# Performance work log

Measured on AMD Instinct MI355X. Metric: run time of the kernel, lower is better.

The kernel has to match this reference:

```python
import jax, jax.numpy as jnp
import numpy as np

D_MODEL = 1024
NUM_HEADS = 16
HEAD_DIM = D_MODEL // NUM_HEADS

def setup_inputs() -> dict:
    key = jax.random.key(0)
    ks = jax.random.split(key, 9)
    B, L = 2, 2048
    s = 1.0 / np.sqrt(D_MODEL)
    return {
        "x":  jax.random.normal(ks[0], (B, L, D_MODEL), dtype=jnp.float32),
        "Wq": jax.random.uniform(ks[1], (D_MODEL, D_MODEL), jnp.float32, -s, s),
        "bq": jax.random.uniform(ks[2], (D_MODEL,), jnp.float32, -s, s),
        "Wk": jax.random.uniform(ks[3], (D_MODEL, D_MODEL), jnp.float32, -s, s),
        "bk": jax.random.uniform(ks[4], (D_MODEL,), jnp.float32, -s, s),
        "Wv": jax.random.uniform(ks[5], (D_MODEL, D_MODEL), jnp.float32, -s, s),
        "bv": jax.random.uniform(ks[6], (D_MODEL,), jnp.float32, -s, s),
        "Wo": jax.random.uniform(ks[7], (D_MODEL, D_MODEL), jnp.float32, -s, s),
        "bo": jax.random.uniform(ks[8], (D_MODEL,), jnp.float32, -s, s),
    }

def _split_heads(t):
    B, L, _ = t.shape
    return t.reshape(B, L, NUM_HEADS, HEAD_DIM).transpose(0, 2, 1, 3)  # [B,H,L,Dh]

def reference(x, Wq, bq, Wk, bk, Wv, bv, Wo, bo):
    # Linear projections (torch Linear: y = x @ W.T + b)
    Q = _split_heads(x @ Wq.T + bq)
    K = _split_heads(x @ Wk.T + bk)
    V = _split_heads(x @ Wv.T + bv)
    scale = 1.0 / jnp.sqrt(jnp.asarray(HEAD_DIM, dtype=x.dtype))
    scores = jnp.einsum('bhqd,bhkd->bhqk', Q, K) * scale  # [B,H,L,L]
    attn_weights = jax.nn.softmax(scores, axis=-1)
    ctx = jnp.einsum('bhqk,bhkd->bhqd', attn_weights, V)  # [B,H,L,Dh]
    B, H, L, Dh = ctx.shape
    ctx = ctx.transpose(0, 2, 1, 3).reshape(B, L, H * Dh)
    out = ctx @ Wo.T + bo  # dropout p=0.0 -> identity
    return (out, attn_weights)
```

## Files before the change

### kernel.cpp

```cpp
#include <hip/hip_runtime.h>

typedef unsigned short u16;
typedef __bf16 bf16x8 __attribute__((ext_vector_type(8)));
typedef float f32x4 __attribute__((ext_vector_type(4)));

#define LSTR 40
#define WSTR 72

__device__ __forceinline__ u16 f2bf(float f) {
    union { float f; unsigned int u; } v; v.f = f;
    unsigned int u = v.u;
    u += 0x7fffu + ((u >> 16) & 1u);
    return (u16)(u >> 16);
}

__device__ __forceinline__ u16 cvt_bf(float f) {
    __bf16 h = (__bf16)f;
    union { __bf16 h; u16 u; } v; v.h = h; return v.u;
}

__device__ __forceinline__ void stage8_bf(const u16* __restrict__ g, u16* __restrict__ lds) {
    *(uint4*)lds = *(const uint4*)g;
}

__device__ __forceinline__ void gload16(const u16* g, u16* l) {
    __builtin_amdgcn_global_load_lds((const __attribute__((address_space(1))) unsigned int*)(const void*)g,
                                     (__attribute__((address_space(3))) unsigned int*)(void*)l, 16, 0, 0);
}

__device__ __forceinline__ void mfma_tile(const u16* lA, const u16* lB,
                                          int wm, int wn, int quad, int m16,
                                          f32x4 (&acc)[2][2]) {
    bf16x8 a0 = *(const bf16x8*)(lA + (wm + m16) * LSTR + quad * 8);
    bf16x8 a1 = *(const bf16x8*)(lA + (wm + 16 + m16) * LSTR + quad * 8);
    bf16x8 b0 = *(const bf16x8*)(lB + (wn + m16) * LSTR + quad * 8);
    bf16x8 b1 = *(const bf16x8*)(lB + (wn + 16 + m16) * LSTR + quad * 8);
    acc[0][0] = __builtin_amdgcn_mfma_f32_16x16x32_bf16(a0, b0, acc[0][0], 0, 0, 0);
    acc[0][1] = __builtin_amdgcn_mfma_f32_16x16x32_bf16(a0, b1, acc[0][1], 0, 0, 0);
    acc[1][0] = __builtin_amdgcn_mfma_f32_16x16x32_bf16(a1, b0, acc[1][0], 0, 0, 0);
    acc[1][1] = __builtin_amdgcn_mfma_f32_16x16x32_bf16(a1, b1, acc[1][1], 0, 0, 0);
}

__global__ __launch_bounds__(256) void k_cvtX(const float* __restrict__ src, u16* __restrict__ dst) {
    const size_t i = ((size_t)blockIdx.x * 256 + threadIdx.x) * 8;
    float4 v0 = *(const float4*)(src + i);
    float4 v1 = *(const float4*)(src + i + 4);
    u16 o[8];
    o[0] = f2bf(v0.x); o[1] = f2bf(v0.y); o[2] = f2bf(v0.z); o[3] = f2bf(v0.w);
    o[4] = f2bf(v1.x); o[5] = f2bf(v1.y); o[6] = f2bf(v1.z); o[7] = f2bf(v1.w);
    *(uint4*)(dst + i) = *(const uint4*)o;
}

__global__ __launch_bounds__(256) void k_cvtW(const float* __restrict__ w0, const float* __restrict__ w1,
                                              const float* __restrict__ w2, const float* __restrict__ w3,
                                              u16* __restrict__ dst) {
    const int z = blockIdx.z;
    const float* src = z == 0 ? w0 : z == 1 ? w1 : z == 2 ? w2 : w3;
    const size_t i = ((size_t)blockIdx.x * 256 + threadIdx.x) * 8;
    float4 v0 = *(const float4*)(src + i);
    float4 v1 = *(const float4*)(src + i + 4);
    u16 o[8];
    o[0] = f2bf(v0.x); o[1] = f2bf(v0.y); o[2] = f2bf(v0.z); o[3] = f2bf(v0.w);
    o[4] = f2bf(v1.x); o[5] = f2bf(v1.y); o[6] = f2bf(v1.z); o[7] = f2bf(v1.w);
    *(uint4*)(dst + (size_t)z * 1048576 + i) = *(const uint4*)o;
}

__global__ __launch_bounds__(256) void k_qkv(const u16* __restrict__ Xb, const u16* __restrict__ Wb,
                                             const float* __restrict__ bq, const float* __restrict__ bk,
                                             const float* __restrict__ bv,
                                             u16* __restrict__ Q, u16* __restrict__ Kd, u16* __restrict__ Vt) {
    __shared__ __align__(16) u16 lA[128 * 32];
    __shared__ __align__(16) u16 lB[128 * 32];
    const int t = threadIdx.x;
    const int n0 = blockIdx.x * 128;
    const int m0 = blockIdx.y * 128;
    const int lane = t & 63, wave = t >> 6;
    const int wm = (wave >> 1) * 64, wn = (wave & 1) * 64;
    const int quad = lane >> 4, m16 = lane & 15;
    const int r4 = t >> 2, c8 = (t & 3) * 8;
    f32x4 acc[4][4] = {};
    for (int k0 = 0; k0 < 1024; k0 += 32) {
        gload16(Xb + (size_t)(m0 + r4) * 1024 + k0 + c8,       &lA[t * 8]);
        gload16(Xb + (size_t)(m0 + 64 + r4) * 1024 + k0 + c8,  &lA[2048 + t * 8]);
        gload16(Wb + (size_t)(n0 + r4) * 1024 + k0 + c8,       &lB[t * 8]);
        gload16(Wb + (size_t)(n0 + 64 + r4) * 1024 + k0 + c8,  &lB[2048 + t * 8]);
        __syncthreads();
        bf16x8 af[4], bfr[4];
#pragma unroll
        for (int i = 0; i < 4; ++i) {
            af[i]  = *(const bf16x8*)(lA + (wm + i * 16 + m16) * 32 + quad * 8);
            bfr[i] = *(const bf16x8*)(lB + (wn + i * 16 + m16) * 32 + quad * 8);
        }
#pragma unroll
        for (int mi = 0; mi < 4; ++mi)
#pragma unroll
            for (int ni = 0; ni < 4; ++ni)
                acc[mi][ni] = __builtin_amdgcn_mfma_f32_16x16x32_bf16(af[mi], bfr[ni], acc[mi][ni], 0, 0, 0);
        __syncthreads();
    }
#pragma unroll
    for (int ni = 0; ni < 4; ++ni) {
        const int gcol = n0 + wn + ni * 16 + m16;
        const int mat = gcol >> 10;
        const int col = gcol & 1023;
        const int h = col >> 6, d = col & 63;
        const float bias = (mat == 0 ? bq : mat == 1 ? bk : bv)[col];
        u16* dst = mat == 0 ? Q : mat == 1 ? Kd : Vt;
#pragma unroll
        for (int mi = 0; mi < 4; ++mi)
#pragma unroll
            for (int e = 0; e < 4; ++e) {
                const int row = m0 + wm + mi * 16 + quad * 4 + e;
                const int b = row >> 11, l = row & 2047;
                const float v = acc[mi][ni][e] + bias;
                size_t idx;
                if (mat == 2) idx = (((size_t)(b * 16 + h)) * 64 + d) * 2048 + l;
                else          idx = (((size_t)(b * 16 + h)) * 2048 + l) * 64 + d;
                dst[idx] = cvt_bf(v);
            }
    }
}

__global__ __launch_bounds__(256) void k_attn(const u16* __restrict__ Q,
                                              const u16* __restrict__ K,
                                              const u16* __restrict__ Vt,
                                              float* __restrict__ attn,
                                              u16* __restrict__ ctx) {
    __shared__ __align__(16) u16 lK[64 * WSTR];
    __shared__ __align__(16) u16 lV[64 * WSTR];
    __shared__ __align__(16) u16 lW[64 * WSTR];
    __shared__ float sred[2][64];
    const int t = threadIdx.x;
    const int bh = blockIdx.y;
    const int m0 = blockIdx.x * 64;
    const int lane = t & 63, wave = t >> 6;
    const int wm = (wave >> 1) * 32, wn = (wave & 1) * 32;
    const int quad = lane >> 4, m16 = lane & 15;
    const int sr = t >> 3, sc = (t & 7) * 8;
    const u16* Qh = Q + (size_t)bh * 2048 * 64;
    const u16* Kh = K + (size_t)bh * 2048 * 64;
    const u16* Vh = Vt + (size_t)bh * 64 * 2048;
    float* ah = attn + ((size_t)bh << 22) + (size_t)m0 * 2048;

    bf16x8 qf[2][2];
#pragma unroll
    for (int mi = 0; mi < 2; ++mi)
#pragma unroll
        for (int ks = 0; ks < 2; ++ks)
            qf[mi][ks] = *(const bf16x8*)(Qh + (size_t)(m0 + wm + mi * 16 + m16) * 64 + ks * 32 + quad * 8);

    float slane[8] = {};

    for (int kt = 0; kt < 32; ++kt) {
        __syncthreads();
        *(uint4*)&lK[sr * WSTR + sc]        = *(const uint4*)(Kh + (size_t)(kt * 64 + sr) * 64 + sc);
        *(uint4*)&lK[(sr + 32) * WSTR + sc] = *(const uint4*)(Kh + (size_t)(kt * 64 + sr + 32) * 64 + sc);
        __syncthreads();
        f32x4 sacc[2][2] = {};
#pragma unroll
        for (int ks = 0; ks < 2; ++ks) {
            bf16x8 b0 = *(const bf16x8*)(lK + (wn + m16) * WSTR + ks * 32 + quad * 8);
            bf16x8 b1 = *(const bf16x8*)(lK + (wn + 16 + m16) * WSTR + ks * 32 + quad * 8);
            sacc[0][0] = __builtin_amdgcn_mfma_f32_16x16x32_bf16(qf[0][ks], b0, sacc[0][0], 0, 0, 0);
            sacc[0][1] = __builtin_amdgcn_mfma_f32_16x16x32_bf16(qf[0][ks], b1, sacc[0][1], 0, 0, 0);
            sacc[1][0] = __builtin_amdgcn_mfma_f32_16x16x32_bf16(qf[1][ks], b0, sacc[1][0], 0, 0, 0);
            sacc[1][1] = __builtin_amdgcn_mfma_f32_16x16x32_bf16(qf[1][ks], b1, sacc[1][1], 0, 0, 0);
        }
#pragma unroll
        for (int mi = 0; mi < 2; ++mi)
#pragma unroll
            for (int e = 0; e < 4; ++e)
                slane[mi * 4 + e] += __expf(sacc[mi][0][e] * 0.125f) + __expf(sacc[mi][1][e] * 0.125f);
    }

#pragma unroll
    for (int i = 0; i < 8; ++i) {
        float s = slane[i];
        s += __shfl_xor(s, 1); s += __shfl_xor(s, 2); s += __shfl_xor(s, 4); s += __shfl_xor(s, 8);
        slane[i] = s;
    }
    if (m16 == 0) {
#pragma unroll
        for (int mi = 0; mi < 2; ++mi)
#pragma unroll
            for (int e = 0; e < 4; ++e)
                sred[wave & 1][wm + mi * 16 + quad * 4 + e] = slane[mi * 4 + e];
    }
    __syncthreads();
    float inv[8];
#pragma unroll
    for (int mi = 0; mi < 2; ++mi)
#pragma unroll
        for (int e = 0; e < 4; ++e) {
            const int row = wm + mi * 16 + quad * 4 + e;
            inv[mi * 4 + e] = 1.0f / (sred[0][row] + sred[1][row]);
        }

    f32x4 cacc[2][2] = {};
    for (int kt = 0; kt < 32; ++kt) {
        __syncthreads();
        *(uint4*)&lK[sr * WSTR + sc]        = *(const uint4*)(Kh + (size_t)(kt * 64 + sr) * 64 + sc);
        *(uint4*)&lK[(sr + 32) * WSTR + sc] = *(const uint4*)(Kh + (size_t)(kt * 64 + sr + 32) * 64 + sc);
        *(uint4*)&lV[sr * WSTR + sc]        = *(const uint4*)(Vh + (size_t)sr * 2048 + kt * 64 + sc);
        *(uint4*)&lV[(sr + 32) * WSTR + sc] = *(const uint4*)(Vh + (size_t)(sr + 32) * 2048 + kt * 64 + sc);
        __syncthreads();
        f32x4 sacc[2][2] = {};
#pragma unroll
        for (int ks = 0; ks < 2; ++ks) {
            bf16x8 b0 = *(const bf16x8*)(lK + (wn + m16) * WSTR + ks * 32 + quad * 8);
            bf16x8 b1 = *(const bf16x8*)(lK + (wn + 16 + m16) * WSTR + ks * 32 + quad * 8);
            sacc[0][0] = __builtin_amdgcn_mfma_f32_16x16x32_bf16(qf[0][ks], b0, sacc[0][0], 0, 0, 0);
            sacc[0][1] = __builtin_amdgcn_mfma_f32_16x16x32_bf16(qf[0][ks], b1, sacc[0][1], 0, 0, 0);
            sacc[1][0] = __builtin_amdgcn_mfma_f32_16x16x32_bf16(qf[1][ks], b0, sacc[1][0], 0, 0, 0);
            sacc[1][1] = __builtin_amdgcn_mfma_f32_16x16x32_bf16(qf[1][ks], b1, sacc[1][1], 0, 0, 0);
        }
#pragma unroll
        for (int mi = 0; mi < 2; ++mi)
#pragma unroll
            for (int ni = 0; ni < 2; ++ni)
#pragma unroll
                for (int e = 0; e < 4; ++e) {
                    const float w = __expf(sacc[mi][ni][e] * 0.125f) * inv[mi * 4 + e];
                    const int row = wm + mi * 16 + quad * 4 + e;
                    const int col = wn + ni * 16 + m16;
                    ah[(size_t)row * 2048 + kt * 64 + col] = w;
                    lW[row * WSTR + col] = cvt_bf(w);
                }
        __syncthreads();
#pragma unroll
        for (int ks = 0; ks < 2; ++ks) {
            bf16x8 a0 = *(const bf16x8*)(lW + (wm + m16) * WSTR + ks * 32 + quad * 8);
            bf16x8 a1 = *(const bf16x8*)(lW + (wm + 16 + m16) * WSTR + ks * 32 + quad * 8);
            bf16x8 b0 = *(const bf16x8*)(lV + (wn + m16) * WSTR + ks * 32 + quad * 8);
            bf16x8 b1 = *(const bf16x8*)(lV + (wn + 16 + m16) * WSTR + ks * 32 + quad * 8);
            cacc[0][0] = __builtin_amdgcn_mfma_f32_16x16x32_bf16(a0, b0, cacc[0][0], 0, 0, 0);
            cacc[0][1] = __builtin_amdgcn_mfma_f32_16x16x32_bf16(a0, b1, cacc[0][1], 0, 0, 0);
            cacc[1][0] = __builtin_amdgcn_mfma_f32_16x16x32_bf16(a1, b0, cacc[1][0], 0, 0, 0);
            cacc[1][1] = __builtin_amdgcn_mfma_f32_16x16x32_bf16(a1, b1, cacc[1][1], 0, 0, 0);
        }
    }

#pragma unroll
    for (int mi = 0; mi < 2; ++mi)
#pragma unroll
        for (int ni = 0; ni < 2; ++ni)
#pragma unroll
            for (int e = 0; e < 4; ++e) {
                const int row = m0 + wm + mi * 16 + quad * 4 + e;
                const int col = wn + ni * 16 + m16;
                ctx[(size_t)bh * 2048 * 64 + (size_t)row * 64 + col] = cvt_bf(cacc[mi][ni][e]);
            }
}

__global__ __launch_bounds__(256) void k_out(const u16* __restrict__ ctx,
                                             const u16* __restrict__ WoB,
                                             const float* __restrict__ bo,
                                             float* __restrict__ out) {
    __shared__ __align__(16) u16 lA[64 * LSTR];
    __shared__ __align__(16) u16 lB[64 * LSTR];
    const int t = threadIdx.x;
    const int n0 = blockIdx.x * 64, m0 = blockIdx.y * 64;
    const int lane = t & 63, wave = t >> 6;
    const int wm = (wave >> 1) * 32, wn = (wave & 1) * 32;
    const int quad = lane >> 4, m16 = lane & 15;
    const int r = t >> 2, c8 = (t & 3) * 8;
    const int m = m0 + r;
    const int b = m >> 11, l = m & 2047;
    f32x4 acc[2][2] = {};
    for (int k0 = 0; k0 < 1024; k0 += 32) {
        const int kk = k0 + c8;
        const int h = kk >> 6, d = kk & 63;
        stage8_bf(ctx + (((size_t)(b * 16 + h) * 2048 + l) * 64 + d), &lA[r * LSTR + c8]);
        stage8_bf(WoB + (size_t)(n0 + r) * 1024 + k0 + c8, &lB[r * LSTR + c8]);
        __syncthreads();
        mfma_tile(lA, lB, wm, wn, quad, m16, acc);
        __syncthreads();
    }
#pragma unroll
    for (int mi = 0; mi < 2; ++mi)
#pragma unroll
        for (int ni = 0; ni < 2; ++ni) {
            const int col = n0 + wn + ni * 16 + m16;
            const float bv = bo[col];
#pragma unroll
            for (int e = 0; e < 4; ++e) {
                const int row = m0 + wm + mi * 16 + quad * 4 + e;
                out[(size_t)row * 1024 + col] = acc[mi][ni][e] + bv;
            }
        }
}

extern "C" void kernel_launch(void* const* d_in, const int* in_sizes, int n_in,
                              void* d_out, int out_size, void* d_ws, size_t ws_size,
                              hipStream_t stream) {
    const float* x  = (const float*)d_in[0];
    const float* Wq = (const float*)d_in[1];
    const float* bq = (const float*)d_in[2];
    const float* Wk = (const float*)d_in[3];
    const float* bk = (const float*)d_in[4];
    const float* Wv = (const float*)d_in[5];
    const float* bv = (const float*)d_in[6];
    const float* Wo = (const float*)d_in[7];
    const float* bo = (const float*)d_in[8];

    float* out_f = (float*)d_out;
    float* attn  = out_f + (size_t)4096 * 1024;

    u16* Xb = (u16*)d_ws;
    u16* Wb = Xb + (size_t)4194304;
    u16* Qb = Wb + (size_t)4194304;
    u16* Kb = Qb + (size_t)4194304;
    u16* Vt = Kb + (size_t)4194304;

    dim3 blk(256);
    k_cvtX<<<dim3(2048), blk, 0, stream>>>(x, Xb);
    k_cvtW<<<dim3(512, 1, 4), blk, 0, stream>>>(Wq, Wk, Wv, Wo, Wb);
    k_qkv<<<dim3(24, 32), blk, 0, stream>>>(Xb, Wb, bq, bk, bv, Qb, Kb, Vt);
    k_attn<<<dim3(32, 32), blk, 0, stream>>>(Qb, Kb, Vt, attn, Qb);
    k_out<<<dim3(16, 64), blk, 0, stream>>>(Qb, Wb + (size_t)3072 * 1024, bo, out_f);
}
```

Measured before the change: 780.3 us.

## Transpose score MFMA so each lane holds four consecutive keys for vector stores

The score MFMA operands are swapped to compute K·Q^T, so each lane's accumulator holds four consecutive key columns of one query row. This lets the fp32 attention-weight writes become 16-byte vector stores and the bf16 LDS writes become 8-byte stores, replacing scattered scalar stores. It also moves the attention store after the barrier, uses exp2 with a folded log2e scale, and simplifies the row-sum reduction to two cross-quad shuffles. Row ownership per wave changes, which adds some index bookkeeping and fixed offset registers.

```diff
diff --git a/kernel.cpp b/kernel.cpp
--- a/kernel.cpp
+++ b/kernel.cpp
@@ -134,6 +134,8 @@
     const int bh = blockIdx.y;
     const int m0 = blockIdx.x * 64;
     const int lane = t & 63, wave = t >> 6;
+    const int wq = (wave & 1) * 32;
+    const int wk = (wave >> 1) * 32;
     const int wm = (wave >> 1) * 32, wn = (wave & 1) * 32;
     const int quad = lane >> 4, m16 = lane & 15;
     const int sr = t >> 3, sc = (t & 7) * 8;
@@ -142,101 +144,120 @@
     const u16* Vh = Vt + (size_t)bh * 64 * 2048;
     float* ah = attn + ((size_t)bh << 22) + (size_t)m0 * 2048;
 
+    const float SC = 0.18033688011112042f;
+
     bf16x8 qf[2][2];
 #pragma unroll
+    for (int ni = 0; ni < 2; ++ni)
+#pragma unroll
+        for (int ks = 0; ks < 2; ++ks)
+            qf[ni][ks] = *(const bf16x8*)(Qh + (size_t)(m0 + wq + ni * 16 + m16) * 64 + ks * 32 + quad * 8);
+
+    float slane[2] = {0.f, 0.f};
+    {
+        const u16* kp = Kh + (size_t)sr * 64 + sc;
+        for (int kt = 0; kt < 32; ++kt) {
+            __syncthreads();
+            *(uint4*)&lK[sr * WSTR + sc]        = *(const uint4*)kp;
+            *(uint4*)&lK[(sr + 32) * WSTR + sc] = *(const uint4*)(kp + 32 * 64);
+            kp += 64 * 64;
+            __syncthreads();
+            f32x4 sacc[2][2] = {};
+#pragma unroll
+            for (int ks = 0; ks < 2; ++ks) {
+                bf16x8 a0 = *(const bf16x8*)(lK + (wk + m16) * WSTR + ks * 32 + quad * 8);
+                bf16x8 a1 = *(const bf16x8*)(lK + (wk + 16 + m16) * WSTR + ks * 32 + quad * 8);
+                sacc[0][0] = __builtin_amdgcn_mfma_f32_16x16x32_bf16(a0, qf[0][ks], sacc[0][0], 0, 0, 0);
+                sacc[0][1] = __builtin_amdgcn_mfma_f32_16x16x32_bf16(a0, qf[1][ks], sacc[0][1], 0, 0, 0);
+                sacc[1][0] = __builtin_amdgcn_mfma_f32_16x16x32_bf16(a1, qf[0][ks], sacc[1][0], 0, 0, 0);
+                sacc[1][1] = __builtin_amdgcn_mfma_f32_16x16x32_bf16(a1, qf[1][ks], sacc[1][1], 0, 0, 0);
+            }
+#pragma unroll
+            for (int mi = 0; mi < 2; ++mi)
+#pragma unroll
+                for (int e = 0; e < 4; ++e) {
+                    slane[0] += __builtin_amdgcn_exp2f(sacc[mi][0][e] * SC);
+                    slane[1] += __builtin_amdgcn_exp2f(sacc[mi][1][e] * SC);
+                }
+        }
+    }
+#pragma unroll
+    for (int ni = 0; ni < 2; ++ni) {
+        slane[ni] += __shfl_xor(slane[ni], 16);
+        slane[ni] += __shfl_xor(slane[ni], 32);
+    }
+    if (quad == 0) {
+        sred[wave >> 1][wq + m16]      = slane[0];
+        sred[wave >> 1][wq + 16 + m16] = slane[1];
+    }
+    __syncthreads();
+    float inv[2];
+    inv[0] = 1.0f / (sred[0][wq + m16]      + sred[1][wq + m16]);
+    inv[1] = 1.0f / (sred[0][wq + 16 + m16] + sred[1][wq + 16 + m16]);
+
+    unsigned aoff[2][2], lwoff[2][2];
+#pragma unroll
     for (int mi = 0; mi < 2; ++mi)
 #pragma unroll
-        for (int ks = 0; ks < 2; ++ks)
-            qf[mi][ks] = *(const bf16x8*)(Qh + (size_t)(m0 + wm + mi * 16 + m16) * 64 + ks * 32 + quad * 8);
-
-    float slane[8] = {};
-
-    for (int kt = 0; kt < 32; ++kt) {
-        __syncthreads();
-        *(uint4*)&lK[sr * WSTR + sc]        = *(const uint4*)(Kh + (size_t)(kt * 64 + sr) * 64 + sc);
-        *(uint4*)&lK[(sr + 32) * WSTR + sc] = *(const uint4*)(Kh + (size_t)(kt * 64 + sr + 32) * 64 + sc);
-        __syncthreads();
-        f32x4 sacc[2][2] = {};
-#pragma unroll
-        for (int ks = 0; ks < 2; ++ks) {
-            bf16x8 b0 = *(const bf16x8*)(lK + (wn + m16) * WSTR + ks * 32 + quad * 8);
-            bf16x8 b1 = *(const bf16x8*)(lK + (wn + 16 + m16) * WSTR + ks * 32 + quad * 8);
-            sacc[0][0] = __builtin_amdgcn_mfma_f32_16x16x32_bf16(qf[0][ks], b0, sacc[0][0], 0, 0, 0);
-            sacc[0][1] = __builtin_amdgcn_mfma_f32_16x16x32_bf16(qf[0][ks], b1, sacc[0][1], 0, 0, 0);
-            sacc[1][0] = __builtin_amdgcn_mfma_f32_16x16x32_bf16(qf[1][ks], b0, sacc[1][0], 0, 0, 0);
-            sacc[1][1] = __builtin_amdgcn_mfma_f32_16x16x32_bf16(qf[1][ks], b1, sacc[1][1], 0, 0, 0);
-        }
-#pragma unroll
-        for (int mi = 0; mi < 2; ++mi)
-#pragma unroll
-            for (int e = 0; e < 4; ++e)
-                slane[mi * 4 + e] += __expf(sacc[mi][0][e] * 0.125f) + __expf(sacc[mi][1][e] * 0.125f);
-    }
-
-#pragma unroll
-    for (int i = 0; i < 8; ++i) {
-        float s = slane[i];
-        s += __shfl_xor(s, 1); s += __shfl_xor(s, 2); s += __shfl_xor(s, 4); s += __shfl_xor(s, 8);
-        slane[i] = s;
-    }
-    if (m16 == 0) {
-#pragma unroll
-        for (int mi = 0; mi < 2; ++mi)
-#pragma unroll
-            for (int e = 0; e < 4; ++e)
-                sred[wave & 1][wm + mi * 16 + quad * 4 + e] = slane[mi * 4 + e];
-    }
-    __syncthreads();
-    float inv[8];
-#pragma unroll
-    for (int mi = 0; mi < 2; ++mi)
-#pragma unroll
-        for (int e = 0; e < 4; ++e) {
-            const int row = wm + mi * 16 + quad * 4 + e;
-            inv[mi * 4 + e] = 1.0f / (sred[0][row] + sred[1][row]);
+        for (int ni = 0; ni < 2; ++ni) {
+            const int q = wq + ni * 16 + m16;
+            const int k = wk + mi * 16 + quad * 4;
+            aoff[mi][ni]  = (unsigned)(q * 2048 + k);
+            lwoff[mi][ni] = (unsigned)(q * WSTR + k);
         }
 
     f32x4 cacc[2][2] = {};
-    for (int kt = 0; kt < 32; ++kt) {
-        __syncthreads();
-        *(uint4*)&lK[sr * WSTR + sc]        = *(const uint4*)(Kh + (size_t)(kt * 64 + sr) * 64 + sc);
-        *(uint4*)&lK[(sr + 32) * WSTR + sc] = *(const uint4*)(Kh + (size_t)(kt * 64 + sr + 32) * 64 + sc);
-        *(uint4*)&lV[sr * WSTR + sc]        = *(const uint4*)(Vh + (size_t)sr * 2048 + kt * 64 + sc);
-        *(uint4*)&lV[(sr + 32) * WSTR + sc] = *(const uint4*)(Vh + (size_t)(sr + 32) * 2048 + kt * 64 + sc);
-        __syncthreads();
-        f32x4 sacc[2][2] = {};
-#pragma unroll
-        for (int ks = 0; ks < 2; ++ks) {
-            bf16x8 b0 = *(const bf16x8*)(lK + (wn + m16) * WSTR + ks * 32 + quad * 8);
-            bf16x8 b1 = *(const bf16x8*)(lK + (wn + 16 + m16) * WSTR + ks * 32 + quad * 8);
-            sacc[0][0] = __builtin_amdgcn_mfma_f32_16x16x32_bf16(qf[0][ks], b0, sacc[0][0], 0, 0, 0);
-            sacc[0][1] = __builtin_amdgcn_mfma_f32_16x16x32_bf16(qf[0][ks], b1, sacc[0][1], 0, 0, 0);
-            sacc[1][0] = __builtin_amdgcn_mfma_f32_16x16x32_bf16(qf[1][ks], b0, sacc[1][0], 0, 0, 0);
-            sacc[1][1] = __builtin_amdgcn_mfma_f32_16x16x32_bf16(qf[1][ks], b1, sacc[1][1], 0, 0, 0);
-        }
-#pragma unroll
-        for (int mi = 0; mi < 2; ++mi)
-#pragma unroll
-            for (int ni = 0; ni < 2; ++ni)
-#pragma unroll
-                for (int e = 0; e < 4; ++e) {
-                    const float w = __expf(sacc[mi][ni][e] * 0.125f) * inv[mi * 4 + e];
-                    const int row = wm + mi * 16 + quad * 4 + e;
-                    const int col = wn + ni * 16 + m16;
-                    ah[(size_t)row * 2048 + kt * 64 + col] = w;
-                    lW[row * WSTR + col] = cvt_bf(w);
+    {
+        const u16* kp = Kh + (size_t)sr * 64 + sc;
+        const u16* vp = Vh + (size_t)sr * 2048 + sc;
+        for (int kt = 0; kt < 32; ++kt) {
+            __syncthreads();
+            *(uint4*)&lK[sr * WSTR + sc]        = *(const uint4*)kp;
+            *(uint4*)&lK[(sr + 32) * WSTR + sc] = *(const uint4*)(kp + 32 * 64);
+            *(uint4*)&lV[sr * WSTR + sc]        = *(const uint4*)vp;
+            *(uint4*)&lV[(sr + 32) * WSTR + sc] = *(const uint4*)(vp + 32 * 2048);
+            kp += 64 * 64; vp += 64;
+            __syncthreads();
+            f32x4 sacc[2][2] = {};
+#pragma unroll
+            for (int ks = 0; ks < 2; ++ks) {
+                bf16x8 a0 = *(const bf16x8*)(lK + (wk + m16) * WSTR + ks * 32 + quad * 8);
+                bf16x8 a1 = *(const bf16x8*)(lK + (wk + 16 + m16) * WSTR + ks * 32 + quad * 8);
+                sacc[0][0] = __builtin_amdgcn_mfma_f32_16x16x32_bf16(a0, qf[0][ks], sacc[0][0], 0, 0, 0);
+                sacc[0][1] = __builtin_amdgcn_mfma_f32_16x16x32_bf16(a0, qf[1][ks], sacc[0][1], 0, 0, 0);
+                sacc[1][0] = __builtin_amdgcn_mfma_f32_16x16x32_bf16(a1, qf[0][ks], sacc[1][0], 0, 0, 0);
+                sacc[1][1] = __builtin_amdgcn_mfma_f32_16x16x32_bf16(a1, qf[1][ks], sacc[1][1], 0, 0, 0);
+            }
+#pragma unroll
+            for (int mi = 0; mi < 2; ++mi)
+#pragma unroll
+                for (int ni = 0; ni < 2; ++ni) {
+#pragma unroll
+                    for (int e = 0; e < 4; ++e)
+                        sacc[mi][ni][e] = __builtin_amdgcn_exp2f(sacc[mi][ni][e] * SC) * inv[ni];
+                    u16 p[4];
+                    p[0] = cvt_bf(sacc[mi][ni][0]); p[1] = cvt_bf(sacc[mi][ni][1]);
+                    p[2] = cvt_bf(sacc[mi][ni][2]); p[3] = cvt_bf(sacc[mi][ni][3]);
+                    *(uint2*)&lW[lwoff[mi][ni]] = *(const uint2*)p;
                 }
-        __syncthreads();
-#pragma unroll
-        for (int ks = 0; ks < 2; ++ks) {
-            bf16x8 a0 = *(const bf16x8*)(lW + (wm + m16) * WSTR + ks * 32 + quad * 8);
-            bf16x8 a1 = *(const bf16x8*)(lW + (wm + 16 + m16) * WSTR + ks * 32 + quad * 8);
-            bf16x8 b0 = *(const bf16x8*)(lV + (wn + m16) * WSTR + ks * 32 + quad * 8);
-            bf16x8 b1 = *(const bf16x8*)(lV + (wn + 16 + m16) * WSTR + ks * 32 + quad * 8);
-            cacc[0][0] = __builtin_amdgcn_mfma_f32_16x16x32_bf16(a0, b0, cacc[0][0], 0, 0, 0);
-            cacc[0][1] = __builtin_amdgcn_mfma_f32_16x16x32_bf16(a0, b1, cacc[0][1], 0, 0, 0);
-            cacc[1][0] = __builtin_amdgcn_mfma_f32_16x16x32_bf16(a1, b0, cacc[1][0], 0, 0, 0);
-            cacc[1][1] = __builtin_amdgcn_mfma_f32_16x16x32_bf16(a1, b1, cacc[1][1], 0, 0, 0);
+            __syncthreads();
+            float* ap = ah + kt * 64;
+#pragma unroll
+            for (int mi = 0; mi < 2; ++mi)
+#pragma unroll
+                for (int ni = 0; ni < 2; ++ni)
+                    *(f32x4*)(ap + aoff[mi][ni]) = sacc[mi][ni];
+#pragma unroll
+            for (int ks = 0; ks < 2; ++ks) {
+                bf16x8 a0 = *(const bf16x8*)(lW + (wm + m16) * WSTR + ks * 32 + quad * 8);
+                bf16x8 a1 = *(const bf16x8*)(lW + (wm + 16 + m16) * WSTR + ks * 32 + quad * 8);
+                bf16x8 b0 = *(const bf16x8*)(lV + (wn + m16) * WSTR + ks * 32 + quad * 8);
+                bf16x8 b1 = *(const bf16x8*)(lV + (wn + 16 + m16) * WSTR + ks * 32 + quad * 8);
+                cacc[0][0] = __builtin_amdgcn_mfma_f32_16x16x32_bf16(a0, b0, cacc[0][0], 0, 0, 0);
+                cacc[0][1] = __builtin_amdgcn_mfma_f32_16x16x32_bf16(a0, b1, cacc[0][1], 0, 0, 0);
+                cacc[1][0] = __builtin_amdgcn_mfma_f32_16x16x32_bf16(a1, b0, cacc[1][0], 0, 0, 0);
+                cacc[1][1] = __builtin_amdgcn_mfma_f32_16x16x32_bf16(a1, b1, cacc[1][1], 0, 0, 0);
+            }
         }
     }
 
```

Measured after the change: 780.2 us. Within noise of the previous version (-0.0%).
